# Kernel tuning notes

Hardware: AMD Instinct MI355X
Metric: run time of the kernel (lower is better)

The kernel has to match this reference:

```python
import jax, jax.numpy as jnp
import numpy as np

N, H, W = 128, 192, 192
THING = 81            # cfg.MODEL.SOGNET.THING_NUM_CLASSES
CLS_DIM = 128         # cls_embedding_dim
POS_DIM = 64          # pos_embedding_dim
REL_DIM = CLS_DIM + POS_DIM


def setup_inputs() -> dict:
    key = jax.random.key(0)
    ks = jax.random.split(key, 8)
    mask_logits = jax.random.normal(ks[0], (1, N, H, W), dtype=jnp.float32)
    # valid boxes: x_max > x_min, y_max > y_min (log(w/h) must be finite)
    xy = jax.random.uniform(ks[1], (N, 2), minval=0.0, maxval=800.0)
    wh = jax.random.uniform(ks[2], (N, 2), minval=16.0, maxval=256.0)
    bbox = jnp.concatenate([xy, xy + wh], axis=1).astype(jnp.float32)
    cls_idx = jax.random.randint(ks[3], (N,), 1, THING)  # values in [1, 80]
    # params (kaiming-normal-ish scale)
    W_U = jax.random.normal(ks[4], (THING - 1, CLS_DIM), jnp.float32) * (2.0 / (THING - 1)) ** 0.5
    W_V = jax.random.normal(ks[5], (THING - 1, CLS_DIM), jnp.float32) * (2.0 / (THING - 1)) ** 0.5
    W_pos = jax.random.normal(ks[6], (4, POS_DIM), jnp.float32) * (2.0 / 4.0) ** 0.5
    W_P = jax.random.normal(ks[7], (REL_DIM, 1), jnp.float32) * (2.0 / REL_DIM) ** 0.5
    return {"mask_logits": mask_logits, "bbox": bbox, "W_U": W_U, "W_V": W_V,
            "W_pos": W_pos, "W_P": W_P, "cls_idx": cls_idx}


def _position_matrix(bbox):
    x_min, y_min, x_max, y_max = bbox[:, 0], bbox[:, 1], bbox[:, 2], bbox[:, 3]
    w = x_max - x_min
    h = y_max - y_min
    x_ctr = (x_min + x_max) / 2.0
    y_ctr = (y_min + y_max) / 2.0
    dx = -(x_ctr[:, None] - x_ctr[None, :]) / w[:, None]          # [N, N]
    dy = -(y_ctr[:, None] - y_ctr[None, :]) / h[:, None]
    dw = jnp.log(w[None, :] / w[:, None])                          # log(w_j / w_i)
    dh = jnp.log(h[None, :] / h[:, None])
    return jnp.stack([dx, dy, dw, dh], axis=2)                     # [N, N, 4]


def reference(mask_logits, bbox, W_U, W_V, W_pos, W_P, cls_idx):
    # --- class relation: outer product of two relu'd class embeddings ---
    one_hot = jax.nn.one_hot(cls_idx - 1, THING - 1, dtype=mask_logits.dtype)  # [N, 80]
    feat1 = jax.nn.relu(one_hot @ W_U)                             # [N, CLS_DIM]
    feat2 = jax.nn.relu(one_hot @ W_V)
    cls_rel = feat1[:, None, :] * feat2[None, :, :]                # [N, N, CLS_DIM]
    # --- position relation: 1x1 conv == linear over last dim ---
    pos_rel = jax.nn.relu(jnp.einsum('ijk,kd->ijd', _position_matrix(bbox), W_pos))  # [N, N, POS_DIM]
    # --- relation score ---
    relation_feat = jnp.concatenate([cls_rel, pos_rel], axis=2)    # [N, N, REL_DIM]
    overlap_score = jax.nn.sigmoid(jnp.einsum('ijk,k->ij', relation_feat, W_P[:, 0]))  # [N, N]
    relation_score = jax.nn.relu(overlap_score - overlap_score.T)  # [N, N]
    # --- relation-weighted mask aggregation ---
    # naive: sum_m (ml*mp)[b,n] * mp[b,m] * score[n,m]  -> factor the m-reduction as a GEMM
    mask_prob = jax.nn.sigmoid(mask_logits)                        # [1, N, H, W]
    weighted = jnp.einsum('nm,bmhw->bnhw', relation_score, mask_prob)
    overlap_part = mask_logits * mask_prob * weighted              # [1, N, H, W]
    return mask_logits - overlap_part
```

## Files before the change

### kernel.cpp

```cpp
#include <hip/hip_runtime.h>

#define HW    36864
#define RST   136

typedef unsigned short u16;
typedef unsigned int   u32;
typedef __attribute__((ext_vector_type(8))) short bf16x8;
typedef __attribute__((ext_vector_type(4))) float f32x4;

__device__ __forceinline__ float bf2f(u32 u) {
    union { u32 i; float f; } c; c.i = u << 16; return c.f;
}
__device__ __forceinline__ u16 f2bf(float f) {
    union { float f; u32 i; } c; c.f = f;
    u32 r = (c.i + 0x7fffu + ((c.i >> 16) & 1u)) >> 16;
    return (u16)r;
}
__device__ __forceinline__ u32 pack2(float a, float b) {
    return (u32)f2bf(a) | ((u32)f2bf(b) << 16);
}
__device__ __forceinline__ float sigf(float x) { return 1.0f / (1.0f + __expf(-x)); }

__device__ __forceinline__ void unpack8(uint4 v, float* o) {
    o[0] = bf2f(v.x & 0xffffu); o[1] = bf2f(v.x >> 16);
    o[2] = bf2f(v.y & 0xffffu); o[3] = bf2f(v.y >> 16);
    o[4] = bf2f(v.z & 0xffffu); o[5] = bf2f(v.z >> 16);
    o[6] = bf2f(v.w & 0xffffu); o[7] = bf2f(v.w >> 16);
}

__device__ __forceinline__ bool is_bf16_blk(const void* ml, int tid) {
    int pred = 0;
    if (tid < 128) {
        u16 v = ((const u16*)ml)[tid];
        u32 e = (v >> 7) & 0xffu;
        pred = ((v & 0x7fffu) == 0 || (e >= 90u && e <= 140u)) ? 1 : 0;
    }
    int cnt = __syncthreads_count(pred);
    return cnt >= 100;
}

__global__ __launch_bounds__(256) void k_rel(
    const void* __restrict__ ml,   const void* __restrict__ bbox,
    const void* __restrict__ WU,   const void* __restrict__ WV,
    const void* __restrict__ Wpos, const void* __restrict__ WP,
    const int* __restrict__ cls,   u16* __restrict__ relN)
{
    const int tid = threadIdx.x;
    const bool bf = is_bf16_blk(ml, tid);
    const int n = blockIdx.x;

    __shared__ float u_s[128], v_s[128], wpos_s[256], wpp_s[64], bbn_s[4];
    __shared__ float d1_s[80], d2_s[80];

    const int cn = cls[n] - 1;
    if (bf) {
        if (tid < 128) {
            float wp = bf2f(((const u16*)WP)[tid]);
            u_s[tid] = fmaxf(bf2f(((const u16*)WU)[cn * 128 + tid]), 0.f) * wp;
            v_s[tid] = fmaxf(bf2f(((const u16*)WV)[cn * 128 + tid]), 0.f) * wp;
        }
        wpos_s[tid] = bf2f(((const u16*)Wpos)[tid]);
        if (tid < 64) wpp_s[tid] = bf2f(((const u16*)WP)[128 + tid]);
        if (tid < 4)  bbn_s[tid] = bf2f(((const u16*)bbox)[n * 4 + tid]);
    } else {
        if (tid < 128) {
            float wp = ((const float*)WP)[tid];
            u_s[tid] = fmaxf(((const float*)WU)[cn * 128 + tid], 0.f) * wp;
            v_s[tid] = fmaxf(((const float*)WV)[cn * 128 + tid], 0.f) * wp;
        }
        wpos_s[tid] = ((const float*)Wpos)[tid];
        if (tid < 64) wpp_s[tid] = ((const float*)WP)[128 + tid];
        if (tid < 4)  bbn_s[tid] = ((const float*)bbox)[n * 4 + tid];
    }
    __syncthreads();

    {
        const int wv_ = tid >> 6, lane = tid & 63;
        const float ua = u_s[lane], ub = u_s[64 + lane];
        const float va = v_s[lane], vb = v_s[64 + lane];
        for (int a = wv_; a < 80; a += 4) {
            float x0, x1, y0, y1;
            if (bf) {
                x0 = bf2f(((const u16*)WV)[a * 128 + lane]);
                x1 = bf2f(((const u16*)WV)[a * 128 + 64 + lane]);
                y0 = bf2f(((const u16*)WU)[a * 128 + lane]);
                y1 = bf2f(((const u16*)WU)[a * 128 + 64 + lane]);
            } else {
                x0 = ((const float*)WV)[a * 128 + lane];
                x1 = ((const float*)WV)[a * 128 + 64 + lane];
                y0 = ((const float*)WU)[a * 128 + lane];
                y1 = ((const float*)WU)[a * 128 + 64 + lane];
            }
            float p1 = ua * fmaxf(x0, 0.f) + ub * fmaxf(x1, 0.f);
            float p2 = va * fmaxf(y0, 0.f) + vb * fmaxf(y1, 0.f);
            #pragma unroll
            for (int o = 32; o; o >>= 1) {
                p1 += __shfl_xor(p1, o);
                p2 += __shfl_xor(p2, o);
            }
            if (lane == 0) { d1_s[a] = p1; d2_s[a] = p2; }
        }
    }
    __syncthreads();

    if (tid >= 128) return;
    const int m = tid;
    const int cm = cls[m] - 1;
    float s1 = d1_s[cm];
    float s2 = d2_s[cm];

    const float xmn = bbn_s[0], ymn = bbn_s[1], xMn = bbn_s[2], yMn = bbn_s[3];
    const float wn = xMn - xmn, hn = yMn - ymn;
    const float xcn = 0.5f * (xmn + xMn), ycn = 0.5f * (ymn + yMn);
    float xmm, ymm, xMm, yMm;
    if (bf) {
        xmm = bf2f(((const u16*)bbox)[m * 4 + 0]); ymm = bf2f(((const u16*)bbox)[m * 4 + 1]);
        xMm = bf2f(((const u16*)bbox)[m * 4 + 2]); yMm = bf2f(((const u16*)bbox)[m * 4 + 3]);
    } else {
        xmm = ((const float*)bbox)[m * 4 + 0]; ymm = ((const float*)bbox)[m * 4 + 1];
        xMm = ((const float*)bbox)[m * 4 + 2]; yMm = ((const float*)bbox)[m * 4 + 3];
    }
    const float wm = xMm - xmm, hm = yMm - ymm;
    const float xcm = 0.5f * (xmm + xMm), ycm = 0.5f * (ymm + yMm);

    const float p0 = -(xcn - xcm) / wn, p1 = -(ycn - ycm) / hn;
    const float p2 = __logf(wm / wn),   p3 = __logf(hm / hn);
    const float q0 = -(xcm - xcn) / wm, q1 = -(ycm - ycn) / hm;
    const float q2 = __logf(wn / wm),   q3 = __logf(hn / hm);

    #pragma unroll 8
    for (int d = 0; d < 64; ++d) {
        float w0 = wpos_s[d], w1 = wpos_s[64 + d], w2 = wpos_s[128 + d], w3 = wpos_s[192 + d];
        float wp = wpp_s[d];
        float t1 = p0 * w0 + p1 * w1 + p2 * w2 + p3 * w3;
        float t2 = q0 * w0 + q1 * w1 + q2 * w2 + q3 * w3;
        s1 += fmaxf(t1, 0.f) * wp;
        s2 += fmaxf(t2, 0.f) * wp;
    }

    float r = fmaxf(sigf(s1) - sigf(s2), 0.f);
    relN[n * 128 + m] = f2bf(r);
}

__global__ __launch_bounds__(256, 2) void k_main(
    const void* __restrict__ mlv, const u16* __restrict__ relN,
    void* __restrict__ outv)
{
    const int tid = threadIdx.x;
    const bool bf = is_bf16_blk(mlv, tid);

    __shared__ u16 rel_s[128 * RST];
    __shared__ u16 prob_s[64 * 64];

    const int px0  = blockIdx.x * 64;
    const int lane = tid & 63;
    const int col  = lane & 15;
    const int quad = lane >> 4;
    const int n0   = (tid >> 6) * 32;

    for (int idx = tid; idx < 2048; idx += 256) {
        int r = idx >> 4, c = idx & 15;
        uint4 v = ((const uint4*)relN)[idx];
        *(uint4*)(rel_s + r * RST + c * 8) = v;
    }

    f32x4 acc[2][4];
    #pragma unroll
    for (int i = 0; i < 2; ++i)
        #pragma unroll
        for (int t = 0; t < 4; ++t) acc[i][t] = (f32x4){0.f, 0.f, 0.f, 0.f};

    for (int h = 0; h < 2; ++h) {
        __syncthreads();
        #pragma unroll
        for (int it = 0; it < 2; ++it) {
            int idx = tid + it * 256;
            int r = idx >> 3, c8 = idx & 7;
            int qr = (r >> 3) & 3;
            size_t base = (size_t)(h * 64 + r) * HW + px0 + c8 * 8;
            float f[8];
            if (bf) {
                uint4 v = *(const uint4*)((const u16*)mlv + base);
                unpack8(v, f);
            } else {
                float4 v0 = *(const float4*)((const float*)mlv + base);
                float4 v1 = *(const float4*)((const float*)mlv + base + 4);
                f[0] = v0.x; f[1] = v0.y; f[2] = v0.z; f[3] = v0.w;
                f[4] = v1.x; f[5] = v1.y; f[6] = v1.z; f[7] = v1.w;
            }
            uint4 o;
            o.x = pack2(sigf(f[0]), sigf(f[1]));
            o.y = pack2(sigf(f[2]), sigf(f[3]));
            o.z = pack2(sigf(f[4]), sigf(f[5]));
            o.w = pack2(sigf(f[6]), sigf(f[7]));
            *(uint4*)((char*)prob_s + r * 128 + ((c8 * 16) ^ (qr * 32))) = o;
        }
        __syncthreads();

        #pragma unroll
        for (int ksl = 0; ksl < 2; ++ksl) {
            const int k0 = h * 64 + ksl * 32 + quad * 8;
            bf16x8 a0 = *(const bf16x8*)(rel_s + (n0 + col) * RST + k0);
            bf16x8 a1 = *(const bf16x8*)(rel_s + (n0 + 16 + col) * RST + k0);
            const int rb = ksl * 32 + quad * 8;
            #pragma unroll
            for (int t = 0; t < 4; ++t) {
                bf16x8 bfrag;
                #pragma unroll
                for (int j = 0; j < 8; ++j) {
                    bfrag[j] = (short)*(const u16*)((const char*)prob_s + (rb + j) * 128
                                                    + ((t * 32 + col * 2) ^ (quad * 32)));
                }
                acc[0][t] = __builtin_amdgcn_mfma_f32_16x16x32_bf16(a0, bfrag, acc[0][t], 0, 0, 0);
                acc[1][t] = __builtin_amdgcn_mfma_f32_16x16x32_bf16(a1, bfrag, acc[1][t], 0, 0, 0);
            }
        }
    }

    #pragma unroll
    for (int i = 0; i < 2; ++i) {
        #pragma unroll
        for (int t = 0; t < 4; ++t) {
            const int nb = n0 + i * 16 + quad * 4;
            const int px = px0 + t * 16 + col;
            #pragma unroll
            for (int r = 0; r < 4; ++r) {
                size_t off = (size_t)(nb + r) * HW + px;
                if (bf) {
                    float mlvv = bf2f((u32)((const u16*)mlv)[off]);
                    float pr = sigf(mlvv);
                    ((u16*)outv)[off] = f2bf(mlvv - mlvv * pr * acc[i][t][r]);
                } else {
                    float mlvv = ((const float*)mlv)[off];
                    float pr = sigf(mlvv);
                    ((float*)outv)[off] = mlvv - mlvv * pr * acc[i][t][r];
                }
            }
        }
    }
}

extern "C" void kernel_launch(void* const* d_in, const int* in_sizes, int n_in,
                              void* d_out, int out_size, void* d_ws, size_t ws_size,
                              hipStream_t stream) {
    const void* ml   = d_in[0];
    const void* bbox = d_in[1];
    const void* WU   = d_in[2];
    const void* WV   = d_in[3];
    const void* Wpos = d_in[4];
    const void* WP   = d_in[5];
    const int*  cls  = (const int*)d_in[6];

    u16* relN = (u16*)d_ws;

    k_rel<<<dim3(128), dim3(256), 0, stream>>>(ml, bbox, WU, WV, Wpos, WP, cls, relN);
    k_main<<<dim3(576), dim3(256), 0, stream>>>(ml, relN, d_out);
}
```

Before: 113.5 us.

## Restructure main kernel: 144-pixel tiles, transposed prob layout, single-pass K

Each block now covers 144 pixels with 512 threads, giving 256 blocks, one per CU, in place of 576. The whole 128-deep sigmoid-prob tile is staged once in a pixel-major transposed LDS layout, so each MFMA B fragment is a single 16-byte vector load rather than eight scalar 16-bit loads. Each wave computes 16 rows against 9 pixel tiles. The cost is that global loads for the prob tile are now strided by HW per element (8 scalar loads per thread with poor coalescing), and the single-wave-per-SIMD occupancy change may reduce latency hiding.

After: 111.7 us. No clear change (-1.6%).

```diff
diff --git a/kernel.cpp b/kernel.cpp
--- a/kernel.cpp
+++ b/kernel.cpp
@@ -1,7 +1,9 @@
 #include <hip/hip_runtime.h>
 
 #define HW    36864
+#define PXT   144
 #define RST   136
+#define PST   136
 
 typedef unsigned short u16;
 typedef unsigned int   u32;
@@ -20,13 +22,6 @@
     return (u32)f2bf(a) | ((u32)f2bf(b) << 16);
 }
 __device__ __forceinline__ float sigf(float x) { return 1.0f / (1.0f + __expf(-x)); }
-
-__device__ __forceinline__ void unpack8(uint4 v, float* o) {
-    o[0] = bf2f(v.x & 0xffffu); o[1] = bf2f(v.x >> 16);
-    o[2] = bf2f(v.y & 0xffffu); o[3] = bf2f(v.y >> 16);
-    o[4] = bf2f(v.z & 0xffffu); o[5] = bf2f(v.z >> 16);
-    o[6] = bf2f(v.w & 0xffffu); o[7] = bf2f(v.w >> 16);
-}
 
 __device__ __forceinline__ bool is_bf16_blk(const void* ml, int tid) {
     int pred = 0;
@@ -142,7 +137,7 @@
     relN[n * 128 + m] = f2bf(r);
 }
 
-__global__ __launch_bounds__(256, 2) void k_main(
+__global__ __launch_bounds__(512) void k_main(
     const void* __restrict__ mlv, const u16* __restrict__ relN,
     void* __restrict__ outv)
 {
@@ -150,91 +145,71 @@
     const bool bf = is_bf16_blk(mlv, tid);
 
     __shared__ u16 rel_s[128 * RST];
-    __shared__ u16 prob_s[64 * 64];
-
-    const int px0  = blockIdx.x * 64;
+    __shared__ u16 prob_t[PXT * PST];
+
+    const int px0  = blockIdx.x * PXT;
     const int lane = tid & 63;
     const int col  = lane & 15;
     const int quad = lane >> 4;
-    const int n0   = (tid >> 6) * 32;
-
-    for (int idx = tid; idx < 2048; idx += 256) {
+    const int n0   = (tid >> 6) * 16;
+
+    for (int idx = tid; idx < 2048; idx += 512) {
         int r = idx >> 4, c = idx & 15;
         uint4 v = ((const uint4*)relN)[idx];
         *(uint4*)(rel_s + r * RST + c * 8) = v;
     }
 
-    f32x4 acc[2][4];
+    for (int u = tid; u < PXT * 16; u += 512) {
+        int px = u % PXT, kg = u / PXT;
+        size_t gbase = (size_t)(kg * 8) * HW + px0 + px;
+        float f[8];
+        if (bf) {
+            #pragma unroll
+            for (int j = 0; j < 8; ++j)
+                f[j] = bf2f((u32)((const u16*)mlv)[gbase + (size_t)j * HW]);
+        } else {
+            #pragma unroll
+            for (int j = 0; j < 8; ++j)
+                f[j] = ((const float*)mlv)[gbase + (size_t)j * HW];
+        }
+        uint4 o;
+        o.x = pack2(sigf(f[0]), sigf(f[1]));
+        o.y = pack2(sigf(f[2]), sigf(f[3]));
+        o.z = pack2(sigf(f[4]), sigf(f[5]));
+        o.w = pack2(sigf(f[6]), sigf(f[7]));
+        *(uint4*)(prob_t + px * PST + kg * 8) = o;
+    }
+    __syncthreads();
+
+    f32x4 acc[9];
     #pragma unroll
-    for (int i = 0; i < 2; ++i)
+    for (int t = 0; t < 9; ++t) acc[t] = (f32x4){0.f, 0.f, 0.f, 0.f};
+
+    #pragma unroll
+    for (int ks = 0; ks < 4; ++ks) {
+        const int k0 = ks * 32 + quad * 8;
+        bf16x8 a = *(const bf16x8*)(rel_s + (n0 + col) * RST + k0);
         #pragma unroll
-        for (int t = 0; t < 4; ++t) acc[i][t] = (f32x4){0.f, 0.f, 0.f, 0.f};
-
-    for (int h = 0; h < 2; ++h) {
-        __syncthreads();
+        for (int t = 0; t < 9; ++t) {
+            bf16x8 b = *(const bf16x8*)(prob_t + (t * 16 + col) * PST + k0);
+            acc[t] = __builtin_amdgcn_mfma_f32_16x16x32_bf16(a, b, acc[t], 0, 0, 0);
+        }
+    }
+
+    #pragma unroll
+    for (int t = 0; t < 9; ++t) {
+        const int px = px0 + t * 16 + col;
         #pragma unroll
-        for (int it = 0; it < 2; ++it) {
-            int idx = tid + it * 256;
-            int r = idx >> 3, c8 = idx & 7;
-            int qr = (r >> 3) & 3;
-            size_t base = (size_t)(h * 64 + r) * HW + px0 + c8 * 8;
-            float f[8];
+        for (int r = 0; r < 4; ++r) {
+            size_t off = (size_t)(n0 + quad * 4 + r) * HW + px;
             if (bf) {
-                uint4 v = *(const uint4*)((const u16*)mlv + base);
-                unpack8(v, f);
+                float mlvv = bf2f((u32)((const u16*)mlv)[off]);
+                float pr = sigf(mlvv);
+                ((u16*)outv)[off] = f2bf(mlvv - mlvv * pr * acc[t][r]);
             } else {
-                float4 v0 = *(const float4*)((const float*)mlv + base);
-                float4 v1 = *(const float4*)((const float*)mlv + base + 4);
-                f[0] = v0.x; f[1] = v0.y; f[2] = v0.z; f[3] = v0.w;
-                f[4] = v1.x; f[5] = v1.y; f[6] = v1.z; f[7] = v1.w;
-            }
-            uint4 o;
-            o.x = pack2(sigf(f[0]), sigf(f[1]));
-            o.y = pack2(sigf(f[2]), sigf(f[3]));
-            o.z = pack2(sigf(f[4]), sigf(f[5]));
-            o.w = pack2(sigf(f[6]), sigf(f[7]));
-            *(uint4*)((char*)prob_s + r * 128 + ((c8 * 16) ^ (qr * 32))) = o;
-        }
-        __syncthreads();
-
-        #pragma unroll
-        for (int ksl = 0; ksl < 2; ++ksl) {
-            const int k0 = h * 64 + ksl * 32 + quad * 8;
-            bf16x8 a0 = *(const bf16x8*)(rel_s + (n0 + col) * RST + k0);
-            bf16x8 a1 = *(const bf16x8*)(rel_s + (n0 + 16 + col) * RST + k0);
-            const int rb = ksl * 32 + quad * 8;
-            #pragma unroll
-            for (int t = 0; t < 4; ++t) {
-                bf16x8 bfrag;
-                #pragma unroll
-                for (int j = 0; j < 8; ++j) {
-                    bfrag[j] = (short)*(const u16*)((const char*)prob_s + (rb + j) * 128
-                                                    + ((t * 32 + col * 2) ^ (quad * 32)));
-                }
-                acc[0][t] = __builtin_amdgcn_mfma_f32_16x16x32_bf16(a0, bfrag, acc[0][t], 0, 0, 0);
-                acc[1][t] = __builtin_amdgcn_mfma_f32_16x16x32_bf16(a1, bfrag, acc[1][t], 0, 0, 0);
-            }
-        }
-    }
-
-    #pragma unroll
-    for (int i = 0; i < 2; ++i) {
-        #pragma unroll
-        for (int t = 0; t < 4; ++t) {
-            const int nb = n0 + i * 16 + quad * 4;
-            const int px = px0 + t * 16 + col;
-            #pragma unroll
-            for (int r = 0; r < 4; ++r) {
-                size_t off = (size_t)(nb + r) * HW + px;
-                if (bf) {
-                    float mlvv = bf2f((u32)((const u16*)mlv)[off]);
-                    float pr = sigf(mlvv);
-                    ((u16*)outv)[off] = f2bf(mlvv - mlvv * pr * acc[i][t][r]);
-                } else {
-                    float mlvv = ((const float*)mlv)[off];
-                    float pr = sigf(mlvv);
-                    ((float*)outv)[off] = mlvv - mlvv * pr * acc[i][t][r];
-                }
+                float mlvv = ((const float*)mlv)[off];
+                float pr = sigf(mlvv);
+                ((float*)outv)[off] = mlvv - mlvv * pr * acc[t][r];
             }
         }
     }
@@ -254,5 +229,5 @@
     u16* relN = (u16*)d_ws;
 
     k_rel<<<dim3(128), dim3(256), 0, stream>>>(ml, bbox, WU, WV, Wpos, WP, cls, relN);
-    k_main<<<dim3(576), dim3(256), 0, stream>>>(ml, relN, d_out);
-}
+    k_main<<<dim3(256), dim3(512), 0, stream>>>(ml, relN, d_out);
+}
```
